# Kernel tuning notes

Measured on AMD Instinct MI355X. Metric: run time of the kernel, lower is better.

The kernel has to match this reference:

```python
import jax, jax.numpy as jnp
import numpy as np


def _next_pow2(n: int) -> int:
    # matches torch: 2 ** ceil(log2(n))
    return 1 << (int(n) - 1).bit_length()


def setup_inputs() -> dict:
    key = jax.random.key(0)
    k1, k2 = jax.random.split(key)
    B, T, L = 256, 32768, 32768
    x = jax.random.normal(k1, (B, T), dtype=jnp.float32)
    filt = jax.random.normal(k2, (1, L), dtype=jnp.float32)
    return {"x": x, "filt": filt}


def reference(x, filt):
    """EpochedFutureFill.forward: exact causal convolution of x with filt.

    The per-token epoched algorithm (tau-step direct sum + FutureFill FFT
    cache refresh every K steps, cache initialized to zero) computes exactly
    y[b, t] = sum_{s=0}^{min(t, L-1)} filt[0, s] * x[b, t-s].
    We compute it with one FFT-based linear convolution, mirroring the
    float32 FFT math of future_fill().
    """
    B, T = x.shape
    L = filt.shape[-1]
    n_fft = _next_pow2(T + L - 1)
    xf = jnp.fft.rfft(x.astype(jnp.float32), n=n_fft)          # (B, n_fft//2+1)
    wf = jnp.fft.rfft(filt.astype(jnp.float32), n=n_fft)       # (1, n_fft//2+1)
    y = jnp.fft.irfft(xf * wf, n=n_fft)[:, :T]                 # causal lags 0..T-1
    return y.astype(x.dtype)
```

## Files before the change

### kernel.cpp

```cpp
#include <hip/hip_runtime.h>
#include <cstdint>

typedef __attribute__((ext_vector_type(8))) short short8;
typedef __attribute__((ext_vector_type(4))) float floatx4;

#define TWO_PI 6.283185307179586f

__device__ __forceinline__ unsigned short f2bf(float f) {
  union { float f; uint32_t u; } c; c.f = f;
  uint32_t u = c.u;
  u += 0x7FFFu + ((u >> 16) & 1u);
  return (unsigned short)(u >> 16);
}
__device__ __forceinline__ uint32_t packbf(float re, float im) {
  return (uint32_t)f2bf(re) | ((uint32_t)f2bf(im) << 16);
}


__device__ __forceinline__ float amat_val(int which, int m, int k) {
  const float w256 = TWO_PI / 256.0f;
  int a = m >> 1, d = m & 1, b = k >> 1, e = k & 1;
  float th = (float)((a * b) & 255) * w256;
  float sn, cs; __sincosf(th, &sn, &cs);
  if (which <= 2) {
    return d == 0 ? (e == 0 ? cs : sn) : (e == 0 ? -sn : cs);
  } else {
    return d == 0 ? (e == 0 ? cs : -sn) : (e == 0 ? sn : cs);
  }
}

__global__ __launch_bounds__(256) void prep_all(
    const float* __restrict__ x, const float* __restrict__ filt,
    unsigned short* __restrict__ A1, unsigned short* __restrict__ A2,
    unsigned short* __restrict__ A3, unsigned short* __restrict__ A4,
    uint32_t* __restrict__ Zp, float2* __restrict__ Gw) {
  const int bid = blockIdx.x;
  const int tid = threadIdx.x;
  if (bid < 3072) {
    int idx = bid * 256 + tid;
    int which, local, KIT;
    unsigned short* dst;
    if (idx < 131072)      { which = 1; local = idx;          KIT = 4; dst = A1; }
    else if (idx < 393216) { which = 2; local = idx - 131072; KIT = 8; dst = A2; }
    else if (idx < 655360) { which = 3; local = idx - 393216; KIT = 8; dst = A3; }
    else                   { which = 4; local = idx - 655360; KIT = 8; dst = A4; }
    int j    = local & 7;
    int lane = (local >> 3) & 63;
    int qlo = lane & 15, qhi = lane >> 4;
    int im   = (local >> 9) & 7;
    int ks   = (local >> 12) & 1;
    int rest = local >> 13;
    int it = rest % KIT, mt = rest / KIT;
    int m = mt * 128 + im * 16 + qlo;
    int k = it * 64 + ks * 32 + qhi * 8 + j;
    dst[local] = f2bf(amat_val(which, m, k));
  } else if (bid < 4096) {
    int b2 = bid - 3072;
    int s = b2 >> 3, rq = b2 & 7;
    const float* x0 = x + (size_t)(2 * s) * 32768;
    const float* x1 = x0 + 32768;
    uint32_t v[16];
    #pragma unroll
    for (int rr = 0; rr < 16; ++rr) {
      int t = tid + 256 * (rq * 16 + rr);
      v[rr] = (uint32_t)f2bf(x0[t]) | ((uint32_t)f2bf(x1[t]) << 16);
    }
    uint32_t* dst = Zp + (size_t)(s * 256 + tid) * 128 + rq * 16;
    #pragma unroll
    for (int j = 0; j < 16; j += 4)
      *(uint4*)(dst + j) = make_uint4(v[j], v[j + 1], v[j + 2], v[j + 3]);
  } else {
    int k1 = bid - 4096, c = tid;
    float ar = 0.f, ai = 0.f;
    for (int r = 0; r < 128; ++r) {
      float v = filt[c + 256 * r];
      float th = (float)((k1 * r) & 255) * (TWO_PI / 256.0f);
      float sn, cs; __sincosf(th, &sn, &cs);
      ar += v * cs; ai -= v * sn;
    }
    float th = (float)((k1 * c) & 65535) * (TWO_PI / 65536.0f);
    float sn, cs; __sincosf(th, &sn, &cs);
    Gw[(k1 << 8) + c] = make_float2(ar * cs + ai * sn, ai * cs - ar * sn);
  }
}

__global__ __launch_bounds__(256) void prep_wb(const float2* __restrict__ Gw,
                                               float2* __restrict__ WtT) {
  int k1 = blockIdx.x, k2 = threadIdx.x;
  float ar = 0.f, ai = 0.f;
  for (int c = 0; c < 256; ++c) {
    float2 g = Gw[(k1 << 8) + c];
    float th = (float)((k2 * c) & 255) * (TWO_PI / 256.0f);
    float sn, cs; __sincosf(th, &sn, &cs);
    ar += g.x * cs + g.y * sn;
    ai += g.y * cs - g.x * sn;
  }
  WtT[(k2 << 8) + k1] = make_float2(ar, ai);
}

template <int MODE, int KITERS>
__global__ __launch_bounds__(256, 2) void dft_stage(
    const unsigned short* __restrict__ Af,
    const unsigned short* __restrict__ Bd,
    uint32_t* __restrict__ outp,
    float* __restrict__ yout,
    const float2* __restrict__ WtT) {
  __shared__ unsigned short Sm[34816];
  constexpr int KP = KITERS * 64;

  const int nt = blockIdx.x & 127;
  const int mt = blockIdx.x >> 7;
  const int n0 = nt * 256;

  const int tid = threadIdx.x;
  const int w = tid >> 6, lane = tid & 63;
  const int qlo = lane & 15, qhi = lane >> 4;
  const int r8 = lane >> 3, pl = lane & 7, sj = pl ^ r8, q3 = qlo & 7;

  floatx4 acc[8][4];
  #pragma unroll
  for (int i = 0; i < 8; ++i)
    #pragma unroll
    for (int j = 0; j < 4; ++j) acc[i][j] = (floatx4){0.f, 0.f, 0.f, 0.f};

  auto issueB = [&](int it, int buf) {
    const int k0 = it * 64;
    unsigned short* Bsb = Sm + buf * 16384;
    #pragma unroll
    for (int q = 0; q < 8; ++q) {
      const int R = w * 64 + q * 8 + r8;
      const unsigned short* gB = Bd + (size_t)(n0 + R) * KP + k0 + sj * 8;
      __builtin_amdgcn_global_load_lds(
          (const __attribute__((address_space(1))) uint32_t*)gB,
          (__attribute__((address_space(3))) uint32_t*)&Bsb[(w * 64 + q * 8) * 64], 16, 0, 0);
    }
  };

  issueB(0, 0);
  for (int it = 0; it < KITERS; ++it) {
    __syncthreads();
    if (it + 1 < KITERS) issueB(it + 1, (it + 1) & 1);
    const unsigned short* Bb = Sm + (it & 1) * 16384;
    const unsigned short* Ab = Af + (size_t)((mt * KITERS + it) * 2) * 8 * 512;
    #pragma unroll
    for (int ks = 0; ks < 2; ++ks) {
      short8 a[8], bb[4];
      #pragma unroll
      for (int im = 0; im < 8; ++im)
        a[im] = *(const short8*)(Ab + ((ks * 8 + im) << 9) + (lane << 3));
      #pragma unroll
      for (int in = 0; in < 4; ++in)
        bb[in] = *(const short8*)&Bb[(w * 64 + in * 16 + qlo) * 64 + (((ks * 4 + qhi) ^ q3) << 3)];
      #pragma unroll
      for (int im = 0; im < 8; ++im)
        #pragma unroll
        for (int in = 0; in < 4; ++in)
          acc[im][in] = __builtin_amdgcn_mfma_f32_16x16x32_bf16(a[im], bb[in], acc[im][in], 0, 0, 0);
    }
  }

  if (MODE == 2) {
    __syncthreads();
    uint32_t* Tr = (uint32_t*)Sm;
    #pragma unroll
    for (int im = 0; im < 8; ++im) {
      #pragma unroll
      for (int in = 0; in < 4; ++in) {
        const int nloc = w * 64 + in * 16 + qlo;
        #pragma unroll
        for (int pp = 0; pp < 2; ++pp) {
          const int mloc = im * 8 + qhi * 2 + pp;
          const int mC = mt * 64 + mloc;
          float re = acc[im][in][2 * pp], iv = acc[im][in][2 * pp + 1];
          float2 wv = WtT[(mC << 8) + nloc];
          float r2 = re * wv.x - iv * wv.y, i2 = re * wv.y + iv * wv.x;
          Tr[nloc * 68 + mloc] = packbf(r2, i2);
        }
      }
    }
    __syncthreads();
    uint32_t* dst = outp + (size_t)((nt << 8) + tid) * 256 + mt * 64;
    const uint32_t* srcp = Tr + tid * 68;
    #pragma unroll
    for (int j = 0; j < 64; j += 4)
      *(uint4*)(dst + j) = *(const uint4*)(srcp + j);
    return;
  }

  #pragma unroll
  for (int im = 0; im < 8; ++im) {
    #pragma unroll
    for (int in = 0; in < 4; ++in) {
      const int nloc = w * 64 + in * 16 + qlo;
      #pragma unroll
      for (int pp = 0; pp < 2; ++pp) {
        const int mC = mt * 64 + im * 8 + qhi * 2 + pp;
        float re = acc[im][in][2 * pp], iv = acc[im][in][2 * pp + 1];
        if (MODE == 1) {
          float th = (float)((mC * nloc) & 65535) * (TWO_PI / 65536.0f);
          float sn, cs; __sincosf(th, &sn, &cs);
          float r2 = re * cs + iv * sn, i2 = iv * cs - re * sn;
          outp[(size_t)((nt << 8) + mC) * 256 + nloc] = packbf(r2, i2);
        } else if (MODE == 3) {
          float th = (float)((mC * nloc) & 65535) * (TWO_PI / 65536.0f);
          float sn, cs; __sincosf(th, &sn, &cs);
          float r2 = re * cs - iv * sn, i2 = iv * cs + re * sn;
          outp[(size_t)((nt << 8) + mC) * 256 + nloc] = packbf(r2, i2);
        } else {
          const float sc = 1.0f / 65536.0f;
          float* y0 = yout + ((size_t)nt << 16) + (mC << 8) + nloc;
          y0[0] = re * sc;
          y0[32768] = iv * sc;
        }
      }
    }
  }
}

extern "C" void kernel_launch(void* const* d_in, const int* in_sizes, int n_in,
                              void* d_out, int out_size, void* d_ws, size_t ws_size,
                              hipStream_t stream) {
  const float* x = (const float*)d_in[0];
  const float* filt = (const float*)d_in[1];
  float* Y = (float*)d_out;

  char* ws = (char*)d_ws;
  unsigned short* A1 = (unsigned short*)(ws + 0);
  unsigned short* A2 = (unsigned short*)(ws + 0x40000);
  unsigned short* A3 = (unsigned short*)(ws + 0xC0000);
  unsigned short* A4 = (unsigned short*)(ws + 0x140000);
  float2* Gw  = (float2*)(ws + 0x180000);
  float2* WtT = (float2*)(ws + 0x200000);
  unsigned short* Zp = (unsigned short*)(ws + (3u << 20));
  unsigned short* G2 = (unsigned short*)(ws + 19922944u);
  unsigned short* P  = (unsigned short*)(ws + 53477376u);
  unsigned short* H2 = (unsigned short*)(ws + (3u << 20));

  hipLaunchKernelGGL(prep_all, dim3(4352), dim3(256), 0, stream,
                     x, filt, A1, A2, A3, A4, (uint32_t*)Zp, Gw);
  hipLaunchKernelGGL(prep_wb, dim3(256), dim3(256), 0, stream, Gw, WtT);

  hipLaunchKernelGGL((dft_stage<1, 4>), dim3(512), dim3(256), 0, stream,
                     A1, Zp, (uint32_t*)G2, (float*)nullptr, (const float2*)nullptr);
  hipLaunchKernelGGL((dft_stage<2, 8>), dim3(512), dim3(256), 0, stream,
                     A2, G2, (uint32_t*)P, (float*)nullptr, WtT);
  hipLaunchKernelGGL((dft_stage<3, 8>), dim3(512), dim3(256), 0, stream,
                     A3, P, (uint32_t*)H2, (float*)nullptr, (const float2*)nullptr);
  hipLaunchKernelGGL((dft_stage<4, 8>), dim3(256), dim3(256), 0, stream,
                     A4, H2, (uint32_t*)nullptr, Y, (const float2*)nullptr);
}
```

Before: 217.6 us.

## Halve DFT stage N-tile to 128, double grid, raise occupancy to three blocks

Each dft_stage block now covers 128 columns instead of 256. This halves the per-wave accumulator tile and the LDS B buffer, and doubles the grid size, with launch bounds raised to allow three blocks per CU. The A fragments for both k-substeps are loaded at the start of each iteration, before the next B prefetch. The MODE 2 transpose drops its padded LDS layout for an XOR-swizzled one, with two threads writing each output row. The aim is more blocks in flight to hide latency on the 256-CU part. The cost is half the B reuse per A load, since A is now re-read twice as often.

```diff
diff --git a/kernel.cpp b/kernel.cpp
--- a/kernel.cpp
+++ b/kernel.cpp
@@ -99,63 +99,72 @@
 }
 
 template <int MODE, int KITERS>
-__global__ __launch_bounds__(256, 2) void dft_stage(
+__global__ __launch_bounds__(256, 3) void dft_stage(
     const unsigned short* __restrict__ Af,
     const unsigned short* __restrict__ Bd,
     uint32_t* __restrict__ outp,
     float* __restrict__ yout,
     const float2* __restrict__ WtT) {
-  __shared__ unsigned short Sm[34816];
+  __shared__ unsigned short Sm[16384];
   constexpr int KP = KITERS * 64;
 
-  const int nt = blockIdx.x & 127;
-  const int mt = blockIdx.x >> 7;
-  const int n0 = nt * 256;
+  const int nt = blockIdx.x & 255;
+  const int mt = blockIdx.x >> 8;
+  const int n0 = nt * 128;
+  const int s_idx = nt >> 1;
+  const int cl0 = (nt & 1) * 128;
 
   const int tid = threadIdx.x;
   const int w = tid >> 6, lane = tid & 63;
   const int qlo = lane & 15, qhi = lane >> 4;
   const int r8 = lane >> 3, pl = lane & 7, sj = pl ^ r8, q3 = qlo & 7;
 
-  floatx4 acc[8][4];
+  floatx4 acc[8][2];
   #pragma unroll
   for (int i = 0; i < 8; ++i)
     #pragma unroll
-    for (int j = 0; j < 4; ++j) acc[i][j] = (floatx4){0.f, 0.f, 0.f, 0.f};
+    for (int j = 0; j < 2; ++j) acc[i][j] = (floatx4){0.f, 0.f, 0.f, 0.f};
 
   auto issueB = [&](int it, int buf) {
     const int k0 = it * 64;
-    unsigned short* Bsb = Sm + buf * 16384;
-    #pragma unroll
-    for (int q = 0; q < 8; ++q) {
-      const int R = w * 64 + q * 8 + r8;
+    unsigned short* Bsb = Sm + buf * 8192;
+    #pragma unroll
+    for (int q = 0; q < 4; ++q) {
+      const int R = w * 32 + q * 8 + r8;
       const unsigned short* gB = Bd + (size_t)(n0 + R) * KP + k0 + sj * 8;
       __builtin_amdgcn_global_load_lds(
           (const __attribute__((address_space(1))) uint32_t*)gB,
-          (__attribute__((address_space(3))) uint32_t*)&Bsb[(w * 64 + q * 8) * 64], 16, 0, 0);
+          (__attribute__((address_space(3))) uint32_t*)&Bsb[(w * 32 + q * 8) * 64], 16, 0, 0);
     }
   };
 
   issueB(0, 0);
+  #pragma unroll 1
   for (int it = 0; it < KITERS; ++it) {
     __syncthreads();
+    const unsigned short* Ab = Af + (size_t)((mt * KITERS + it) * 2) * 8 * 512;
+    short8 a0[8], a1[8];
+    #pragma unroll
+    for (int im = 0; im < 8; ++im)
+      a0[im] = *(const short8*)(Ab + (im << 9) + (lane << 3));
+    #pragma unroll
+    for (int im = 0; im < 8; ++im)
+      a1[im] = *(const short8*)(Ab + ((8 + im) << 9) + (lane << 3));
     if (it + 1 < KITERS) issueB(it + 1, (it + 1) & 1);
-    const unsigned short* Bb = Sm + (it & 1) * 16384;
-    const unsigned short* Ab = Af + (size_t)((mt * KITERS + it) * 2) * 8 * 512;
+
+    const unsigned short* Bb = Sm + (it & 1) * 8192;
     #pragma unroll
     for (int ks = 0; ks < 2; ++ks) {
-      short8 a[8], bb[4];
-      #pragma unroll
-      for (int im = 0; im < 8; ++im)
-        a[im] = *(const short8*)(Ab + ((ks * 8 + im) << 9) + (lane << 3));
-      #pragma unroll
-      for (int in = 0; in < 4; ++in)
-        bb[in] = *(const short8*)&Bb[(w * 64 + in * 16 + qlo) * 64 + (((ks * 4 + qhi) ^ q3) << 3)];
+      short8 bb[2];
+      #pragma unroll
+      for (int in = 0; in < 2; ++in)
+        bb[in] = *(const short8*)&Bb[(w * 32 + in * 16 + qlo) * 64 + (((ks * 4 + qhi) ^ q3) << 3)];
       #pragma unroll
       for (int im = 0; im < 8; ++im)
         #pragma unroll
-        for (int in = 0; in < 4; ++in)
-          acc[im][in] = __builtin_amdgcn_mfma_f32_16x16x32_bf16(a[im], bb[in], acc[im][in], 0, 0, 0);
+        for (int in = 0; in < 2; ++in)
+          acc[im][in] = __builtin_amdgcn_mfma_f32_16x16x32_bf16(
+              ks == 0 ? a0[im] : a1[im], bb[in], acc[im][in], 0, 0, 0);
     }
   }
 
@@ -165,50 +174,54 @@
     #pragma unroll
     for (int im = 0; im < 8; ++im) {
       #pragma unroll
-      for (int in = 0; in < 4; ++in) {
-        const int nloc = w * 64 + in * 16 + qlo;
+      for (int in = 0; in < 2; ++in) {
+        const int nloc = w * 32 + in * 16 + qlo;
         #pragma unroll
         for (int pp = 0; pp < 2; ++pp) {
           const int mloc = im * 8 + qhi * 2 + pp;
           const int mC = mt * 64 + mloc;
           float re = acc[im][in][2 * pp], iv = acc[im][in][2 * pp + 1];
-          float2 wv = WtT[(mC << 8) + nloc];
+          float2 wv = WtT[(mC << 8) + cl0 + nloc];
           float r2 = re * wv.x - iv * wv.y, i2 = re * wv.y + iv * wv.x;
-          Tr[nloc * 68 + mloc] = packbf(r2, i2);
+          Tr[nloc * 64 + (mloc ^ ((nloc & 7) << 2))] = packbf(r2, i2);
         }
       }
     }
     __syncthreads();
-    uint32_t* dst = outp + (size_t)((nt << 8) + tid) * 256 + mt * 64;
-    const uint32_t* srcp = Tr + tid * 68;
-    #pragma unroll
-    for (int j = 0; j < 64; j += 4)
-      *(uint4*)(dst + j) = *(const uint4*)(srcp + j);
+    const int ln = tid >> 1, half = tid & 1;
+    const int xorv = (ln & 7) << 2;
+    uint32_t* dst = outp + (size_t)((s_idx << 8) + cl0 + ln) * 256 + mt * 64 + half * 32;
+    #pragma unroll
+    for (int j = 0; j < 32; j += 4) {
+      uint4 v = *(const uint4*)(Tr + ln * 64 + ((half * 32 + j) ^ xorv));
+      *(uint4*)(dst + j) = v;
+    }
     return;
   }
 
   #pragma unroll
   for (int im = 0; im < 8; ++im) {
     #pragma unroll
-    for (int in = 0; in < 4; ++in) {
-      const int nloc = w * 64 + in * 16 + qlo;
+    for (int in = 0; in < 2; ++in) {
+      const int nloc = w * 32 + in * 16 + qlo;
+      const int cloc = cl0 + nloc;
       #pragma unroll
       for (int pp = 0; pp < 2; ++pp) {
         const int mC = mt * 64 + im * 8 + qhi * 2 + pp;
         float re = acc[im][in][2 * pp], iv = acc[im][in][2 * pp + 1];
         if (MODE == 1) {
-          float th = (float)((mC * nloc) & 65535) * (TWO_PI / 65536.0f);
+          float th = (float)((mC * cloc) & 65535) * (TWO_PI / 65536.0f);
           float sn, cs; __sincosf(th, &sn, &cs);
           float r2 = re * cs + iv * sn, i2 = iv * cs - re * sn;
-          outp[(size_t)((nt << 8) + mC) * 256 + nloc] = packbf(r2, i2);
+          outp[(size_t)((s_idx << 8) + mC) * 256 + cloc] = packbf(r2, i2);
         } else if (MODE == 3) {
-          float th = (float)((mC * nloc) & 65535) * (TWO_PI / 65536.0f);
+          float th = (float)((mC * cloc) & 65535) * (TWO_PI / 65536.0f);
           float sn, cs; __sincosf(th, &sn, &cs);
           float r2 = re * cs - iv * sn, i2 = iv * cs + re * sn;
-          outp[(size_t)((nt << 8) + mC) * 256 + nloc] = packbf(r2, i2);
+          outp[(size_t)((s_idx << 8) + mC) * 256 + cloc] = packbf(r2, i2);
         } else {
           const float sc = 1.0f / 65536.0f;
-          float* y0 = yout + ((size_t)nt << 16) + (mC << 8) + nloc;
+          float* y0 = yout + ((size_t)s_idx << 16) + (mC << 8) + cloc;
           y0[0] = re * sc;
           y0[32768] = iv * sc;
         }
@@ -240,12 +253,12 @@
                      x, filt, A1, A2, A3, A4, (uint32_t*)Zp, Gw);
   hipLaunchKernelGGL(prep_wb, dim3(256), dim3(256), 0, stream, Gw, WtT);
 
-  hipLaunchKernelGGL((dft_stage<1, 4>), dim3(512), dim3(256), 0, stream,
+  hipLaunchKernelGGL((dft_stage<1, 4>), dim3(1024), dim3(256), 0, stream,
                      A1, Zp, (uint32_t*)G2, (float*)nullptr, (const float2*)nullptr);
-  hipLaunchKernelGGL((dft_stage<2, 8>), dim3(512), dim3(256), 0, stream,
+  hipLaunchKernelGGL((dft_stage<2, 8>), dim3(1024), dim3(256), 0, stream,
                      A2, G2, (uint32_t*)P, (float*)nullptr, WtT);
-  hipLaunchKernelGGL((dft_stage<3, 8>), dim3(512), dim3(256), 0, stream,
+  hipLaunchKernelGGL((dft_stage<3, 8>), dim3(1024), dim3(256), 0, stream,
                      A3, P, (uint32_t*)H2, (float*)nullptr, (const float2*)nullptr);
-  hipLaunchKernelGGL((dft_stage<4, 8>), dim3(256), dim3(256), 0, stream,
+  hipLaunchKernelGGL((dft_stage<4, 8>), dim3(512), dim3(256), 0, stream,
                      A4, H2, (uint32_t*)nullptr, Y, (const float2*)nullptr);
 }
```

After: 214.6 us. About the same (-1.3%).

## Restructure DFT GEMM stages into N-panel blocks with whole-K B tile in LDS

Applied to the files above, without the earlier changes.

Each block now owns a 64-column panel and loads its entire K extent of B into LDS once, with an XOR swizzle. The double-buffered K loop over 256-wide tiles is gone. Waves split the M dimension, and the A operand is read straight from global memory and cached. The last stage uses 512 blocks instead of 256 by halving its M rows per wave. This removes per-iteration barriers and gives better parallelism, but each block does less work per B load, and holding the full K of B in LDS raises shared-memory use and may limit occupancy.

```diff
diff --git a/kernel.cpp b/kernel.cpp
--- a/kernel.cpp
+++ b/kernel.cpp
@@ -98,117 +98,131 @@
   WtT[(k2 << 8) + k1] = make_float2(ar, ai);
 }
 
-template <int MODE, int KITERS>
-__global__ __launch_bounds__(256, 2) void dft_stage(
+template <int MODE, int KSTEPS, int MR>
+__global__ __launch_bounds__(256, 2) void dft_panel(
     const unsigned short* __restrict__ Af,
     const unsigned short* __restrict__ Bd,
     uint32_t* __restrict__ outp,
     float* __restrict__ yout,
     const float2* __restrict__ WtT) {
-  __shared__ unsigned short Sm[34816];
-  constexpr int KP = KITERS * 64;
-
-  const int nt = blockIdx.x & 127;
-  const int mt = blockIdx.x >> 7;
-  const int n0 = nt * 256;
+  constexpr int KP = KSTEPS * 32;
+  __shared__ unsigned short Bs[64 * KP];
+
+  const int n0 = blockIdx.x * 64;
+  const int s_idx = n0 >> 8;
+  const int cl0 = n0 & 255;
 
   const int tid = threadIdx.x;
   const int w = tid >> 6, lane = tid & 63;
   const int qlo = lane & 15, qhi = lane >> 4;
-  const int r8 = lane >> 3, pl = lane & 7, sj = pl ^ r8, q3 = qlo & 7;
-
-  floatx4 acc[8][4];
-  #pragma unroll
-  for (int i = 0; i < 8; ++i)
-    #pragma unroll
-    for (int j = 0; j < 4; ++j) acc[i][j] = (floatx4){0.f, 0.f, 0.f, 0.f};
-
-  auto issueB = [&](int it, int buf) {
-    const int k0 = it * 64;
-    unsigned short* Bsb = Sm + buf * 16384;
-    #pragma unroll
-    for (int q = 0; q < 8; ++q) {
-      const int R = w * 64 + q * 8 + r8;
-      const unsigned short* gB = Bd + (size_t)(n0 + R) * KP + k0 + sj * 8;
+
+  if (KP == 512) {
+    #pragma unroll
+    for (int rr = 0; rr < 16; ++rr) {
+      const int n = w * 16 + rr;
+      const unsigned short* gB = Bd + (size_t)(n0 + n) * KP + ((lane ^ (n & 7)) << 3);
       __builtin_amdgcn_global_load_lds(
           (const __attribute__((address_space(1))) uint32_t*)gB,
-          (__attribute__((address_space(3))) uint32_t*)&Bsb[(w * 64 + q * 8) * 64], 16, 0, 0);
-    }
-  };
-
-  issueB(0, 0);
-  for (int it = 0; it < KITERS; ++it) {
-    __syncthreads();
-    if (it + 1 < KITERS) issueB(it + 1, (it + 1) & 1);
-    const unsigned short* Bb = Sm + (it & 1) * 16384;
-    const unsigned short* Ab = Af + (size_t)((mt * KITERS + it) * 2) * 8 * 512;
-    #pragma unroll
-    for (int ks = 0; ks < 2; ++ks) {
-      short8 a[8], bb[4];
-      #pragma unroll
-      for (int im = 0; im < 8; ++im)
-        a[im] = *(const short8*)(Ab + ((ks * 8 + im) << 9) + (lane << 3));
+          (__attribute__((address_space(3))) uint32_t*)&Bs[n * KP], 16, 0, 0);
+    }
+  } else {
+    #pragma unroll
+    for (int rr = 0; rr < 8; ++rr) {
+      const int nb = w * 16 + rr * 2;
+      const int n = nb + (lane >> 5);
+      const unsigned short* gB =
+          Bd + (size_t)(n0 + n) * KP + ((((lane & 31) ^ (n & 7))) << 3);
+      __builtin_amdgcn_global_load_lds(
+          (const __attribute__((address_space(1))) uint32_t*)gB,
+          (__attribute__((address_space(3))) uint32_t*)&Bs[nb * KP], 16, 0, 0);
+    }
+  }
+
+  floatx4 acc[MR][4];
+  #pragma unroll
+  for (int i = 0; i < MR; ++i)
+    #pragma unroll
+    for (int j = 0; j < 4; ++j) acc[i][j] = (floatx4){0.f, 0.f, 0.f, 0.f};
+
+  __syncthreads();
+
+  const int fb = w * MR;
+  const unsigned short* At =
+      Af + ((size_t)((fb >> 3) * KSTEPS * 8 + (fb & 7))) * 512 + (lane << 3);
+
+  #pragma unroll 4
+  for (int t = 0; t < KSTEPS; ++t) {
+    short8 a[MR];
+    #pragma unroll
+    for (int i = 0; i < MR; ++i)
+      a[i] = *(const short8*)(At + (size_t)(t * 8 + i) * 512);
+    short8 b[4];
+    #pragma unroll
+    for (int in = 0; in < 4; ++in) {
+      const int n = in * 16 + qlo;
+      const int c = (t * 4 + qhi) ^ (n & 7);
+      b[in] = *(const short8*)&Bs[n * KP + (c << 3)];
+    }
+    #pragma unroll
+    for (int i = 0; i < MR; ++i)
       #pragma unroll
       for (int in = 0; in < 4; ++in)
-        bb[in] = *(const short8*)&Bb[(w * 64 + in * 16 + qlo) * 64 + (((ks * 4 + qhi) ^ q3) << 3)];
-      #pragma unroll
-      for (int im = 0; im < 8; ++im)
-        #pragma unroll
-        for (int in = 0; in < 4; ++in)
-          acc[im][in] = __builtin_amdgcn_mfma_f32_16x16x32_bf16(a[im], bb[in], acc[im][in], 0, 0, 0);
-    }
+        acc[i][in] = __builtin_amdgcn_mfma_f32_16x16x32_bf16(a[i], b[in], acc[i][in], 0, 0, 0);
   }
 
   if (MODE == 2) {
     __syncthreads();
-    uint32_t* Tr = (uint32_t*)Sm;
-    #pragma unroll
-    for (int im = 0; im < 8; ++im) {
+    uint32_t* Tr = (uint32_t*)Bs;
+    #pragma unroll
+    for (int im = 0; im < MR; ++im) {
       #pragma unroll
       for (int in = 0; in < 4; ++in) {
-        const int nloc = w * 64 + in * 16 + qlo;
+        const int nloc = in * 16 + qlo;
         #pragma unroll
         for (int pp = 0; pp < 2; ++pp) {
-          const int mloc = im * 8 + qhi * 2 + pp;
-          const int mC = mt * 64 + mloc;
+          const int mC = (fb + im) * 8 + qhi * 2 + pp;
           float re = acc[im][in][2 * pp], iv = acc[im][in][2 * pp + 1];
-          float2 wv = WtT[(mC << 8) + nloc];
+          float2 wv = WtT[(mC << 8) + cl0 + nloc];
           float r2 = re * wv.x - iv * wv.y, i2 = re * wv.y + iv * wv.x;
-          Tr[nloc * 68 + mloc] = packbf(r2, i2);
+          Tr[nloc * 256 + (mC ^ ((nloc & 7) << 2))] = packbf(r2, i2);
         }
       }
     }
     __syncthreads();
-    uint32_t* dst = outp + (size_t)((nt << 8) + tid) * 256 + mt * 64;
-    const uint32_t* srcp = Tr + tid * 68;
-    #pragma unroll
-    for (int j = 0; j < 64; j += 4)
-      *(uint4*)(dst + j) = *(const uint4*)(srcp + j);
+    const int n = tid >> 2, q = tid & 3;
+    const int xorv = (n & 7) << 2;
+    uint32_t* dst = outp + (size_t)((s_idx << 8) + cl0 + n) * 256 + q * 64;
+    #pragma unroll
+    for (int j = 0; j < 64; j += 4) {
+      uint4 v = *(const uint4*)(Tr + n * 256 + ((q * 64 + j) ^ xorv));
+      *(uint4*)(dst + j) = v;
+    }
     return;
   }
 
   #pragma unroll
-  for (int im = 0; im < 8; ++im) {
+  for (int im = 0; im < MR; ++im) {
     #pragma unroll
     for (int in = 0; in < 4; ++in) {
-      const int nloc = w * 64 + in * 16 + qlo;
+      const int nloc = in * 16 + qlo;
+      const int cloc = cl0 + nloc;
       #pragma unroll
       for (int pp = 0; pp < 2; ++pp) {
-        const int mC = mt * 64 + im * 8 + qhi * 2 + pp;
+        const int mC = (fb + im) * 8 + qhi * 2 + pp;
         float re = acc[im][in][2 * pp], iv = acc[im][in][2 * pp + 1];
         if (MODE == 1) {
-          float th = (float)((mC * nloc) & 65535) * (TWO_PI / 65536.0f);
+          float th = (float)((mC * cloc) & 65535) * (TWO_PI / 65536.0f);
           float sn, cs; __sincosf(th, &sn, &cs);
           float r2 = re * cs + iv * sn, i2 = iv * cs - re * sn;
-          outp[(size_t)((nt << 8) + mC) * 256 + nloc] = packbf(r2, i2);
+          outp[(size_t)((s_idx << 8) + mC) * 256 + cloc] = packbf(r2, i2);
         } else if (MODE == 3) {
-          float th = (float)((mC * nloc) & 65535) * (TWO_PI / 65536.0f);
+          float th = (float)((mC * cloc) & 65535) * (TWO_PI / 65536.0f);
           float sn, cs; __sincosf(th, &sn, &cs);
           float r2 = re * cs - iv * sn, i2 = iv * cs + re * sn;
-          outp[(size_t)((nt << 8) + mC) * 256 + nloc] = packbf(r2, i2);
+          outp[(size_t)((s_idx << 8) + mC) * 256 + cloc] = packbf(r2, i2);
         } else {
           const float sc = 1.0f / 65536.0f;
-          float* y0 = yout + ((size_t)nt << 16) + (mC << 8) + nloc;
+          float* y0 = yout + ((size_t)s_idx << 16) + (mC << 8) + cloc;
           y0[0] = re * sc;
           y0[32768] = iv * sc;
         }
@@ -240,12 +254,12 @@
                      x, filt, A1, A2, A3, A4, (uint32_t*)Zp, Gw);
   hipLaunchKernelGGL(prep_wb, dim3(256), dim3(256), 0, stream, Gw, WtT);
 
-  hipLaunchKernelGGL((dft_stage<1, 4>), dim3(512), dim3(256), 0, stream,
+  hipLaunchKernelGGL((dft_panel<1, 8, 8>), dim3(512), dim3(256), 0, stream,
                      A1, Zp, (uint32_t*)G2, (float*)nullptr, (const float2*)nullptr);
-  hipLaunchKernelGGL((dft_stage<2, 8>), dim3(512), dim3(256), 0, stream,
+  hipLaunchKernelGGL((dft_panel<2, 16, 8>), dim3(512), dim3(256), 0, stream,
                      A2, G2, (uint32_t*)P, (float*)nullptr, WtT);
-  hipLaunchKernelGGL((dft_stage<3, 8>), dim3(512), dim3(256), 0, stream,
+  hipLaunchKernelGGL((dft_panel<3, 16, 8>), dim3(512), dim3(256), 0, stream,
                      A3, P, (uint32_t*)H2, (float*)nullptr, (const float2*)nullptr);
-  hipLaunchKernelGGL((dft_stage<4, 8>), dim3(256), dim3(256), 0, stream,
+  hipLaunchKernelGGL((dft_panel<4, 16, 4>), dim3(512), dim3(256), 0, stream,
                      A4, H2, (uint32_t*)nullptr, Y, (const float2*)nullptr);
 }
```

New measurement: 239.8 us. +10.2%, slower.
